# Kernel optimization log

Measured on AMD Instinct MI355X. Metric: run time of the kernel, lower is better.

Reference implementation:

```python
import jax, jax.numpy as jnp
import numpy as np

EMBED_DIM = 768
NUM_HEADS = 12
HEAD_DIM = EMBED_DIM // NUM_HEADS  # 64
SCALE = HEAD_DIM ** 0.5  # NOTE: source MULTIPLIES by sqrt(head_dim) (likely a bug, kept faithful)


def setup_inputs() -> dict:
    key = jax.random.key(0)
    kx, kq, kk, kv, ko = jax.random.split(key, 5)
    B, N, E = 8, 2048, EMBED_DIM
    s = 1.0 / np.sqrt(E)
    return {
        "x": jax.random.normal(kx, (B, N, E), dtype=jnp.float32),
        # nn.Linear weights stored [out_features, in_features], y = x @ W.T
        "Wq": jax.random.normal(kq, (E, E), dtype=jnp.float32) * s,
        "Wk": jax.random.normal(kk, (E, E), dtype=jnp.float32) * s,
        "Wv": jax.random.normal(kv, (E, E), dtype=jnp.float32) * s,
        "Wo": jax.random.normal(ko, (E, E), dtype=jnp.float32) * s,
    }


def reference(x, Wq, Wk, Wv, Wo):
    # Projections (no bias)
    q = jnp.einsum("bne,fe->bnf", x, Wq)
    k = jnp.einsum("bne,fe->bnf", x, Wk)
    v = jnp.einsum("bne,fe->bnf", x, Wv)
    # Full-width attention over the entire embedding dim (no head split, per source)
    energy = jnp.einsum("bid,bjd->bij", q, k) * SCALE  # [B, N, N]
    attn = jax.nn.softmax(energy, axis=-1)
    out = jnp.einsum("bij,bjd->bid", attn, v)  # [B, N, E]
    return jnp.einsum("bne,fe->bnf", out, Wo)
```

## Files before the change

kernel.cpp:

```cpp
#include <hip/hip_runtime.h>
#include <stdint.h>

typedef __bf16 bf16;
typedef __bf16 bf16x4 __attribute__((ext_vector_type(4)));
typedef __bf16 bf16x8 __attribute__((ext_vector_type(8)));
typedef float  f32x4  __attribute__((ext_vector_type(4)));

constexpr int BB = 8;
constexpr int NN = 2048;
constexpr int EE = 768;
constexpr int MM = BB * NN;
constexpr int E2 = 2 * EE;

typedef const __attribute__((address_space(1))) void* as1_cvp;
typedef __attribute__((address_space(3))) void* as3_vp;

static __device__ __forceinline__ void gld16(const void* g, void* l) {
  __builtin_amdgcn_global_load_lds((as1_cvp)g, (as3_vp)l, 16, 0, 0);
}

__global__ __launch_bounds__(256) void k_splitx(const float4* __restrict__ x,
                                                bf16x4* __restrict__ hi,
                                                bf16x4* __restrict__ lo, int n4) {
  int i = blockIdx.x * 256 + threadIdx.x;
  int st = gridDim.x * 256;
  for (; i < n4; i += st) {
    float4 v = x[i];
    bf16x4 h, l;
    h[0] = (bf16)v.x; l[0] = (bf16)(v.x - (float)h[0]);
    h[1] = (bf16)v.y; l[1] = (bf16)(v.y - (float)h[1]);
    h[2] = (bf16)v.z; l[2] = (bf16)(v.z - (float)h[2]);
    h[3] = (bf16)v.w; l[3] = (bf16)(v.w - (float)h[3]);
    hi[i] = h; lo[i] = l;
  }
}

__global__ __launch_bounds__(256) void k_wprep(const float4* __restrict__ wq,
                                               const float4* __restrict__ wk,
                                               const float4* __restrict__ wv,
                                               const float4* __restrict__ wo,
                                               bf16x4* __restrict__ qkh, bf16x4* __restrict__ qkl,
                                               bf16x4* __restrict__ vb,  bf16x4* __restrict__ ob) {
  const int n4 = EE * EE / 4;
  int sel = blockIdx.y;
  int i = blockIdx.x * 256 + threadIdx.x;
  int st = gridDim.x * 256;
  for (; i < n4; i += st) {
    if (sel <= 1) {
      float4 v = sel == 0 ? wq[i] : wk[i];
      bf16x4 h, l;
      h[0] = (bf16)v.x; l[0] = (bf16)(v.x - (float)h[0]);
      h[1] = (bf16)v.y; l[1] = (bf16)(v.y - (float)h[1]);
      h[2] = (bf16)v.z; l[2] = (bf16)(v.z - (float)h[2]);
      h[3] = (bf16)v.w; l[3] = (bf16)(v.w - (float)h[3]);
      int o = i + sel * n4;
      qkh[o] = h; qkl[o] = l;
    } else {
      float4 v = sel == 2 ? wv[i] : wo[i];
      bf16x4 h;
      h[0] = (bf16)v.x; h[1] = (bf16)v.y; h[2] = (bf16)v.z; h[3] = (bf16)v.w;
      if (sel == 2) vb[i] = h; else ob[i] = h;
    }
  }
}

template <bool SPLIT, int EPI>
__global__ __launch_bounds__(256, 2) void k_gemm(
    const bf16* __restrict__ Ah, const bf16* __restrict__ Al,
    const bf16* __restrict__ Bh, const bf16* __restrict__ Bl,
    void* __restrict__ C0, void* __restrict__ C1,
    int Kdim, int lda, int ldb, int ldc,
    long long sA, long long sB, long long sC, float cscale) {
  constexpr int NTILES = SPLIT ? 4 : 2;
  __shared__ __align__(16) bf16 sm[NTILES * 128 * 64];
  bf16* smAh = sm;
  bf16* smBh = sm + 128 * 64;
  bf16* smAl = SPLIT ? sm + 2 * 128 * 64 : nullptr;
  bf16* smBl = SPLIT ? sm + 3 * 128 * 64 : nullptr;

  const int tid = threadIdx.x;
  const int lane = tid & 63, wid = tid >> 6;
  const int lr = lane & 15, lq = lane >> 4;
  const int wr = (wid >> 1) * 64, wc = (wid & 1) * 64;
  const long long bz = blockIdx.z;
  const int col0 = blockIdx.x * 128, row0 = blockIdx.y * 128;

  const bf16* pAh = Ah + bz * sA;
  const bf16* pBh = Bh + bz * sB;
  const bf16* pAl = SPLIT ? (Al + bz * sA) : nullptr;
  const bf16* pBl = SPLIT ? (Bl + bz * sB) : nullptr;

  f32x4 acc[4][4] = {};

  for (int kt = 0; kt < Kdim; kt += 64) {
    {
      int o = tid * 16;
#pragma unroll
      for (int r = 0; r < 4; r++, o += 4096) {
        int row = o >> 7;
        int c = (o & 127) ^ ((row & 7) << 4);
        gld16((const char*)(pAh + (size_t)(row0 + row) * lda + kt) + c, (char*)smAh + o);
        gld16((const char*)(pBh + (size_t)(col0 + row) * ldb + kt) + c, (char*)smBh + o);
        if constexpr (SPLIT) {
          gld16((const char*)(pAl + (size_t)(row0 + row) * lda + kt) + c, (char*)smAl + o);
          gld16((const char*)(pBl + (size_t)(col0 + row) * ldb + kt) + c, (char*)smBl + o);
        }
      }
    }
    __syncthreads();
#pragma unroll
    for (int kk = 0; kk < 2; kk++) {
      bf16x8 ah[4], bh[4], al[4], bl[4];
#pragma unroll
      for (int i = 0; i < 4; i++) {
        int ar = wr + i * 16 + lr;
        int ao = ar * 128 + ((kk * 64 + lq * 16) ^ ((ar & 7) << 4));
        ah[i] = *(const bf16x8*)((const char*)smAh + ao);
        int br = wc + i * 16 + lr;
        int bo = br * 128 + ((kk * 64 + lq * 16) ^ ((br & 7) << 4));
        bh[i] = *(const bf16x8*)((const char*)smBh + bo);
        if constexpr (SPLIT) {
          al[i] = *(const bf16x8*)((const char*)smAl + ao);
          bl[i] = *(const bf16x8*)((const char*)smBl + bo);
        }
      }
#pragma unroll
      for (int i = 0; i < 4; i++)
#pragma unroll
        for (int j = 0; j < 4; j++) {
          acc[i][j] = __builtin_amdgcn_mfma_f32_16x16x32_bf16(ah[i], bh[j], acc[i][j], 0, 0, 0);
          if constexpr (SPLIT) {
            acc[i][j] = __builtin_amdgcn_mfma_f32_16x16x32_bf16(ah[i], bl[j], acc[i][j], 0, 0, 0);
            acc[i][j] = __builtin_amdgcn_mfma_f32_16x16x32_bf16(al[i], bh[j], acc[i][j], 0, 0, 0);
          }
        }
    }
    __syncthreads();
  }

#pragma unroll
  for (int i = 0; i < 4; i++) {
#pragma unroll
    for (int j2 = 0; j2 < 4; j2++) {
      f32x4 v = acc[i][j2];
      if constexpr (EPI == 3) {
        int r0 = row0 + wr + i * 16 + lq * 4;
        int c = col0 + wc + j2 * 16 + lr;
        int b = r0 >> 11, n0 = r0 & 2047;
        bf16x4 t;
#pragma unroll
        for (int j = 0; j < 4; j++) t[j] = (bf16)(v[j] * cscale);
        *(bf16x4*)((bf16*)C0 + ((size_t)b * EE + c) * NN + n0) = t;
      } else {
#pragma unroll
        for (int j = 0; j < 4; j++) {
          size_t r = (size_t)(row0 + wr + i * 16 + lq * 4 + j);
          size_t c = (size_t)(col0 + wc + j2 * 16 + lr);
          size_t idx = r * (size_t)ldc + c;
          float val = v[j] * cscale;
          if constexpr (EPI == 0) {
            bf16* Chp = (bf16*)C0 + bz * sC;
            bf16* Clp = (bf16*)C1 + bz * sC;
            bf16 h = (bf16)val;
            Chp[idx] = h;
            Clp[idx] = (bf16)(val - (float)h);
          } else if constexpr (EPI == 1) {
            float* Cp = (float*)C0 + bz * sC;
            Cp[idx] = val;
          } else {
            bf16* Cp = (bf16*)C0 + bz * sC;
            Cp[idx] = (bf16)val;
          }
        }
      }
    }
  }
}

__global__ __launch_bounds__(256) void k_softmax(float* __restrict__ S) {
  size_t row = blockIdx.x;
  float* srow = S + row * (size_t)NN;
  int tid = threadIdx.x;
  int wid = tid >> 6, lane = tid & 63;
  const float4* s4 = (const float4*)srow;
  float4 v0 = s4[tid * 2], v1 = s4[tid * 2 + 1];
  float vv[8] = {v0.x, v0.y, v0.z, v0.w, v1.x, v1.y, v1.z, v1.w};
  float m = vv[0];
#pragma unroll
  for (int j = 1; j < 8; j++) m = fmaxf(m, vv[j]);
#pragma unroll
  for (int d = 1; d < 64; d <<= 1) m = fmaxf(m, __shfl_xor(m, d));
  __shared__ float red[8];
  if (lane == 0) red[wid] = m;
  __syncthreads();
  m = fmaxf(fmaxf(red[0], red[1]), fmaxf(red[2], red[3]));
  float e[8];
  float ssum = 0.f;
#pragma unroll
  for (int j = 0; j < 8; j++) { e[j] = __expf(vv[j] - m); ssum += e[j]; }
#pragma unroll
  for (int d = 1; d < 64; d <<= 1) ssum += __shfl_xor(ssum, d);
  if (lane == 0) red[4 + wid] = ssum;
  __syncthreads();
  ssum = red[4] + red[5] + red[6] + red[7];
  float inv = 1.0f / ssum;
  bf16x8 p;
#pragma unroll
  for (int j = 0; j < 8; j++) p[j] = (bf16)(e[j] * inv);
  *(bf16x8*)((bf16*)srow + tid * 8) = p;
}

extern "C" void kernel_launch(void* const* d_in, const int* in_sizes, int n_in,
                              void* d_out, int out_size, void* d_ws, size_t ws_size,
                              hipStream_t stream) {
  const float* x  = (const float*)d_in[0];
  const float* Wq = (const float*)d_in[1];
  const float* Wk = (const float*)d_in[2];
  const float* Wv = (const float*)d_in[3];
  const float* Wo = (const float*)d_in[4];
  float* out = (float*)d_out;
  char* ws = (char*)d_ws;

  const size_t szXE = (size_t)MM * EE * 2;
  const size_t szWb = (size_t)EE * EE * 2;
  const size_t szQKh = (size_t)MM * E2 * 2;
  const size_t szS1 = (size_t)NN * NN * 4;

  bf16* xhi = (bf16*)(ws);
  bf16* xlo = (bf16*)(ws + szXE);
  char* wb  = ws + 2 * szXE;
  bf16* wqkh = (bf16*)(wb);
  bf16* wqkl = (bf16*)(wb + 2 * szWb);
  bf16* wvb  = (bf16*)(wb + 4 * szWb);
  bf16* wob  = (bf16*)(wb + 5 * szWb);
  char* qkb = wb + 6 * szWb;
  bf16* QKh = (bf16*)(qkb);
  bf16* QKl = (bf16*)(qkb + szQKh);
  bf16* Vt  = (bf16*)(qkb + 2 * szQKh);
  char* Sb  = qkb + 2 * szQKh + szXE;
  float* S  = (float*)Sb;
  bf16* Ao  = (bf16*)ws;

  size_t oS = (size_t)(Sb - ws);
  size_t avail = ws_size > oS ? ws_size - oS : 0;
  int G = 8;
  while (G > 1 && (size_t)G * szS1 > avail) G >>= 1;

  k_splitx<<<2048, 256, 0, stream>>>((const float4*)x, (bf16x4*)xhi, (bf16x4*)xlo, MM * EE / 4);
  k_wprep<<<dim3(144, 4), 256, 0, stream>>>((const float4*)Wq, (const float4*)Wk,
                                            (const float4*)Wv, (const float4*)Wo,
                                            (bf16x4*)wqkh, (bf16x4*)wqkl, (bf16x4*)wvb, (bf16x4*)wob);

  k_gemm<true, 0><<<dim3(E2 / 128, MM / 128, 1), 256, 0, stream>>>(
      xhi, xlo, wqkh, wqkl, QKh, QKl, EE, EE, EE, E2, 0, 0, 0, 1.0f);
  k_gemm<false, 3><<<dim3(EE / 128, MM / 128, 1), 256, 0, stream>>>(
      xhi, nullptr, wvb, nullptr, Vt, nullptr, EE, EE, EE, 0, 0, 0, 0, 1.0f);

  const long long sQK = (long long)NN * E2;
  for (int g = 0; g < BB; g += G) {
    const bf16* Qh = QKh + (size_t)g * NN * E2;
    const bf16* Ql = QKl + (size_t)g * NN * E2;
    k_gemm<true, 1><<<dim3(NN / 128, NN / 128, G), 256, 0, stream>>>(
        Qh, Ql, Qh + EE, Ql + EE, S, nullptr, EE, E2, E2, NN,
        sQK, sQK, (long long)NN * NN, 8.0f);
    k_softmax<<<G * NN, 256, 0, stream>>>(S);
    k_gemm<false, 2><<<dim3(EE / 128, NN / 128, G), 256, 0, stream>>>(
        (const bf16*)S, nullptr, Vt + (size_t)g * EE * NN, nullptr,
        Ao + (size_t)g * NN * EE, nullptr, NN, 2 * NN, NN, EE,
        2LL * NN * NN, (long long)EE * NN, (long long)NN * EE, 1.0f);
  }

  k_gemm<false, 1><<<dim3(EE / 128, MM / 128, 1), 256, 0, stream>>>(
      Ao, nullptr, wob, nullptr, out, nullptr, EE, EE, EE, EE, 0, 0, 0, 1.0f);
}
```

Baseline: 448.8 us.

## Template GEMM on K-tile and occupancy; compute V^T by operand swap

```diff
diff --git a/kernel.cpp b/kernel.cpp
--- a/kernel.cpp
+++ b/kernel.cpp
@@ -64,19 +64,21 @@
   }
 }
 
-template <bool SPLIT, int EPI>
-__global__ __launch_bounds__(256, 2) void k_gemm(
+template <bool SPLIT, int EPI, int BK, int LB>
+__global__ __launch_bounds__(256, LB) void k_gemm(
     const bf16* __restrict__ Ah, const bf16* __restrict__ Al,
     const bf16* __restrict__ Bh, const bf16* __restrict__ Bl,
     void* __restrict__ C0, void* __restrict__ C1,
     int Kdim, int lda, int ldb, int ldc,
     long long sA, long long sB, long long sC, float cscale) {
   constexpr int NTILES = SPLIT ? 4 : 2;
-  __shared__ __align__(16) bf16 sm[NTILES * 128 * 64];
-  bf16* smAh = sm;
-  bf16* smBh = sm + 128 * 64;
-  bf16* smAl = SPLIT ? sm + 2 * 128 * 64 : nullptr;
-  bf16* smBl = SPLIT ? sm + 3 * 128 * 64 : nullptr;
+  constexpr int ROWB = BK * 2;
+  constexpr int TILEB = 128 * ROWB;
+  __shared__ __align__(16) bf16 smm[NTILES * 128 * BK];
+  char* smAh = (char*)smm;
+  char* smBh = (char*)smm + TILEB;
+  char* smAl = SPLIT ? (char*)smm + 2 * TILEB : nullptr;
+  char* smBl = SPLIT ? (char*)smm + 3 * TILEB : nullptr;
 
   const int tid = threadIdx.x;
   const int lane = tid & 63, wid = tid >> 6;
@@ -92,36 +94,44 @@
 
   f32x4 acc[4][4] = {};
 
-  for (int kt = 0; kt < Kdim; kt += 64) {
+  for (int kt = 0; kt < Kdim; kt += BK) {
     {
       int o = tid * 16;
 #pragma unroll
-      for (int r = 0; r < 4; r++, o += 4096) {
-        int row = o >> 7;
-        int c = (o & 127) ^ ((row & 7) << 4);
-        gld16((const char*)(pAh + (size_t)(row0 + row) * lda + kt) + c, (char*)smAh + o);
-        gld16((const char*)(pBh + (size_t)(col0 + row) * ldb + kt) + c, (char*)smBh + o);
+      for (int r = 0; r < BK / 16; r++, o += 4096) {
+        int row = o / ROWB;
+        int c;
+        if constexpr (BK == 64) c = (o & (ROWB - 1)) ^ ((row & 7) << 4);
+        else                    c = (o & (ROWB - 1)) ^ (((row ^ (row >> 2)) & 3) << 4);
+        gld16((const char*)(pAh + (size_t)(row0 + row) * lda + kt) + c, smAh + o);
+        gld16((const char*)(pBh + (size_t)(col0 + row) * ldb + kt) + c, smBh + o);
         if constexpr (SPLIT) {
-          gld16((const char*)(pAl + (size_t)(row0 + row) * lda + kt) + c, (char*)smAl + o);
-          gld16((const char*)(pBl + (size_t)(col0 + row) * ldb + kt) + c, (char*)smBl + o);
+          gld16((const char*)(pAl + (size_t)(row0 + row) * lda + kt) + c, smAl + o);
+          gld16((const char*)(pBl + (size_t)(col0 + row) * ldb + kt) + c, smBl + o);
         }
       }
     }
     __syncthreads();
 #pragma unroll
-    for (int kk = 0; kk < 2; kk++) {
+    for (int kk = 0; kk < BK / 32; kk++) {
       bf16x8 ah[4], bh[4], al[4], bl[4];
 #pragma unroll
       for (int i = 0; i < 4; i++) {
         int ar = wr + i * 16 + lr;
-        int ao = ar * 128 + ((kk * 64 + lq * 16) ^ ((ar & 7) << 4));
-        ah[i] = *(const bf16x8*)((const char*)smAh + ao);
         int br = wc + i * 16 + lr;
-        int bo = br * 128 + ((kk * 64 + lq * 16) ^ ((br & 7) << 4));
-        bh[i] = *(const bf16x8*)((const char*)smBh + bo);
+        int ao, bo;
+        if constexpr (BK == 64) {
+          ao = ar * ROWB + ((kk * 64 + lq * 16) ^ ((ar & 7) << 4));
+          bo = br * ROWB + ((kk * 64 + lq * 16) ^ ((br & 7) << 4));
+        } else {
+          ao = ar * ROWB + ((lq * 16) ^ (((ar ^ (ar >> 2)) & 3) << 4));
+          bo = br * ROWB + ((lq * 16) ^ (((br ^ (br >> 2)) & 3) << 4));
+        }
+        ah[i] = *(const bf16x8*)(smAh + ao);
+        bh[i] = *(const bf16x8*)(smBh + bo);
         if constexpr (SPLIT) {
-          al[i] = *(const bf16x8*)((const char*)smAl + ao);
-          bl[i] = *(const bf16x8*)((const char*)smBl + bo);
+          al[i] = *(const bf16x8*)(smAl + ao);
+          bl[i] = *(const bf16x8*)(smBl + bo);
         }
       }
 #pragma unroll
@@ -143,34 +153,24 @@
 #pragma unroll
     for (int j2 = 0; j2 < 4; j2++) {
       f32x4 v = acc[i][j2];
-      if constexpr (EPI == 3) {
-        int r0 = row0 + wr + i * 16 + lq * 4;
-        int c = col0 + wc + j2 * 16 + lr;
-        int b = r0 >> 11, n0 = r0 & 2047;
-        bf16x4 t;
-#pragma unroll
-        for (int j = 0; j < 4; j++) t[j] = (bf16)(v[j] * cscale);
-        *(bf16x4*)((bf16*)C0 + ((size_t)b * EE + c) * NN + n0) = t;
-      } else {
-#pragma unroll
-        for (int j = 0; j < 4; j++) {
-          size_t r = (size_t)(row0 + wr + i * 16 + lq * 4 + j);
-          size_t c = (size_t)(col0 + wc + j2 * 16 + lr);
-          size_t idx = r * (size_t)ldc + c;
-          float val = v[j] * cscale;
-          if constexpr (EPI == 0) {
-            bf16* Chp = (bf16*)C0 + bz * sC;
-            bf16* Clp = (bf16*)C1 + bz * sC;
-            bf16 h = (bf16)val;
-            Chp[idx] = h;
-            Clp[idx] = (bf16)(val - (float)h);
-          } else if constexpr (EPI == 1) {
-            float* Cp = (float*)C0 + bz * sC;
-            Cp[idx] = val;
-          } else {
-            bf16* Cp = (bf16*)C0 + bz * sC;
-            Cp[idx] = (bf16)val;
-          }
+#pragma unroll
+      for (int j = 0; j < 4; j++) {
+        size_t r = (size_t)(row0 + wr + i * 16 + lq * 4 + j);
+        size_t c = (size_t)(col0 + wc + j2 * 16 + lr);
+        size_t idx = r * (size_t)ldc + c;
+        float val = v[j] * cscale;
+        if constexpr (EPI == 0) {
+          bf16* Chp = (bf16*)C0 + bz * sC;
+          bf16* Clp = (bf16*)C1 + bz * sC;
+          bf16 h = (bf16)val;
+          Chp[idx] = h;
+          Clp[idx] = (bf16)(val - (float)h);
+        } else if constexpr (EPI == 1) {
+          float* Cp = (float*)C0 + bz * sC;
+          Cp[idx] = val;
+        } else {
+          bf16* Cp = (bf16*)C0 + bz * sC;
+          Cp[idx] = (bf16)val;
         }
       }
     }
@@ -251,25 +251,25 @@
                                             (const float4*)Wv, (const float4*)Wo,
                                             (bf16x4*)wqkh, (bf16x4*)wqkl, (bf16x4*)wvb, (bf16x4*)wob);
 
-  k_gemm<true, 0><<<dim3(E2 / 128, MM / 128, 1), 256, 0, stream>>>(
+  k_gemm<true, 0, 64, 2><<<dim3(E2 / 128, MM / 128, 1), 256, 0, stream>>>(
       xhi, xlo, wqkh, wqkl, QKh, QKl, EE, EE, EE, E2, 0, 0, 0, 1.0f);
-  k_gemm<false, 3><<<dim3(EE / 128, MM / 128, 1), 256, 0, stream>>>(
-      xhi, nullptr, wvb, nullptr, Vt, nullptr, EE, EE, EE, 0, 0, 0, 0, 1.0f);
+  k_gemm<false, 2, 64, 4><<<dim3(MM / 128, EE / 128, 1), 256, 0, stream>>>(
+      wvb, nullptr, xhi, nullptr, Vt, nullptr, EE, EE, EE, MM, 0, 0, 0, 1.0f);
 
   const long long sQK = (long long)NN * E2;
   for (int g = 0; g < BB; g += G) {
     const bf16* Qh = QKh + (size_t)g * NN * E2;
     const bf16* Ql = QKl + (size_t)g * NN * E2;
-    k_gemm<true, 1><<<dim3(NN / 128, NN / 128, G), 256, 0, stream>>>(
+    k_gemm<true, 1, 32, 4><<<dim3(NN / 128, NN / 128, G), 256, 0, stream>>>(
         Qh, Ql, Qh + EE, Ql + EE, S, nullptr, EE, E2, E2, NN,
         sQK, sQK, (long long)NN * NN, 8.0f);
     k_softmax<<<G * NN, 256, 0, stream>>>(S);
-    k_gemm<false, 2><<<dim3(EE / 128, NN / 128, G), 256, 0, stream>>>(
-        (const bf16*)S, nullptr, Vt + (size_t)g * EE * NN, nullptr,
-        Ao + (size_t)g * NN * EE, nullptr, NN, 2 * NN, NN, EE,
-        2LL * NN * NN, (long long)EE * NN, (long long)NN * EE, 1.0f);
-  }
-
-  k_gemm<false, 1><<<dim3(EE / 128, MM / 128, 1), 256, 0, stream>>>(
+    k_gemm<false, 2, 64, 4><<<dim3(EE / 128, NN / 128, G), 256, 0, stream>>>(
+        (const bf16*)S, nullptr, Vt + (size_t)g * NN, nullptr,
+        Ao + (size_t)g * NN * EE, nullptr, NN, 2 * NN, MM, EE,
+        2LL * NN * NN, (long long)NN, (long long)NN * EE, 1.0f);
+  }
+
+  k_gemm<false, 1, 64, 4><<<dim3(EE / 128, MM / 128, 1), 256, 0, stream>>>(
       Ao, nullptr, wob, nullptr, out, nullptr, EE, EE, EE, EE, 0, 0, 0, 1.0f);
 }
```

After: 465.6 us. 3.7% more time.

## Fold output projection into V weights via precomputed Wo·Wv product

Applied to the files above, without the earlier changes.

```diff
diff --git a/kernel.cpp b/kernel.cpp
--- a/kernel.cpp
+++ b/kernel.cpp
@@ -37,10 +37,9 @@
 
 __global__ __launch_bounds__(256) void k_wprep(const float4* __restrict__ wq,
                                                const float4* __restrict__ wk,
-                                               const float4* __restrict__ wv,
                                                const float4* __restrict__ wo,
                                                bf16x4* __restrict__ qkh, bf16x4* __restrict__ qkl,
-                                               bf16x4* __restrict__ vb,  bf16x4* __restrict__ ob) {
+                                               bf16x4* __restrict__ ob) {
   const int n4 = EE * EE / 4;
   int sel = blockIdx.y;
   int i = blockIdx.x * 256 + threadIdx.x;
@@ -56,11 +55,35 @@
       int o = i + sel * n4;
       qkh[o] = h; qkl[o] = l;
     } else {
-      float4 v = sel == 2 ? wv[i] : wo[i];
+      float4 v = wo[i];
       bf16x4 h;
       h[0] = (bf16)v.x; h[1] = (bf16)v.y; h[2] = (bf16)v.z; h[3] = (bf16)v.w;
-      if (sel == 2) vb[i] = h; else ob[i] = h;
-    }
+      ob[i] = h;
+    }
+  }
+}
+
+__global__ __launch_bounds__(256) void k_wtrans(const float* __restrict__ src,
+                                                bf16* __restrict__ dst) {
+  __shared__ float t[64][65];
+  int e0 = blockIdx.x * 64, f0 = blockIdx.y * 64;
+  int tid = threadIdx.x;
+#pragma unroll
+  for (int h = 0; h < 4; h++) {
+    int lin = h * 1024 + tid * 4;
+    int r = lin >> 6, c = lin & 63;
+    float4 v = *(const float4*)(src + (size_t)(f0 + r) * EE + e0 + c);
+    t[r][c] = v.x; t[r][c + 1] = v.y; t[r][c + 2] = v.z; t[r][c + 3] = v.w;
+  }
+  __syncthreads();
+#pragma unroll
+  for (int h = 0; h < 4; h++) {
+    int lin = h * 1024 + tid * 4;
+    int er = lin >> 6, fc = lin & 63;
+    bf16x4 o;
+#pragma unroll
+    for (int j = 0; j < 4; j++) o[j] = (bf16)t[fc + j][er];
+    *(bf16x4*)(dst + (size_t)(e0 + er) * EE + f0 + fc) = o;
   }
 }
 
@@ -72,11 +95,11 @@
     int Kdim, int lda, int ldb, int ldc,
     long long sA, long long sB, long long sC, float cscale) {
   constexpr int NTILES = SPLIT ? 4 : 2;
-  __shared__ __align__(16) bf16 sm[NTILES * 128 * 64];
-  bf16* smAh = sm;
-  bf16* smBh = sm + 128 * 64;
-  bf16* smAl = SPLIT ? sm + 2 * 128 * 64 : nullptr;
-  bf16* smBl = SPLIT ? sm + 3 * 128 * 64 : nullptr;
+  __shared__ __align__(16) bf16 smm[NTILES * 128 * 64];
+  bf16* smAh = smm;
+  bf16* smBh = smm + 128 * 64;
+  bf16* smAl = SPLIT ? smm + 2 * 128 * 64 : nullptr;
+  bf16* smBl = SPLIT ? smm + 3 * 128 * 64 : nullptr;
 
   const int tid = threadIdx.x;
   const int lane = tid & 63, wid = tid >> 6;
@@ -143,34 +166,24 @@
 #pragma unroll
     for (int j2 = 0; j2 < 4; j2++) {
       f32x4 v = acc[i][j2];
-      if constexpr (EPI == 3) {
-        int r0 = row0 + wr + i * 16 + lq * 4;
-        int c = col0 + wc + j2 * 16 + lr;
-        int b = r0 >> 11, n0 = r0 & 2047;
-        bf16x4 t;
-#pragma unroll
-        for (int j = 0; j < 4; j++) t[j] = (bf16)(v[j] * cscale);
-        *(bf16x4*)((bf16*)C0 + ((size_t)b * EE + c) * NN + n0) = t;
-      } else {
-#pragma unroll
-        for (int j = 0; j < 4; j++) {
-          size_t r = (size_t)(row0 + wr + i * 16 + lq * 4 + j);
-          size_t c = (size_t)(col0 + wc + j2 * 16 + lr);
-          size_t idx = r * (size_t)ldc + c;
-          float val = v[j] * cscale;
-          if constexpr (EPI == 0) {
-            bf16* Chp = (bf16*)C0 + bz * sC;
-            bf16* Clp = (bf16*)C1 + bz * sC;
-            bf16 h = (bf16)val;
-            Chp[idx] = h;
-            Clp[idx] = (bf16)(val - (float)h);
-          } else if constexpr (EPI == 1) {
-            float* Cp = (float*)C0 + bz * sC;
-            Cp[idx] = val;
-          } else {
-            bf16* Cp = (bf16*)C0 + bz * sC;
-            Cp[idx] = (bf16)val;
-          }
+#pragma unroll
+      for (int j = 0; j < 4; j++) {
+        size_t r = (size_t)(row0 + wr + i * 16 + lq * 4 + j);
+        size_t c = (size_t)(col0 + wc + j2 * 16 + lr);
+        size_t idx = r * (size_t)ldc + c;
+        float val = v[j] * cscale;
+        if constexpr (EPI == 0) {
+          bf16* Chp = (bf16*)C0 + bz * sC;
+          bf16* Clp = (bf16*)C1 + bz * sC;
+          bf16 h = (bf16)val;
+          Chp[idx] = h;
+          Clp[idx] = (bf16)(val - (float)h);
+        } else if constexpr (EPI == 1) {
+          float* Cp = (float*)C0 + bz * sC;
+          Cp[idx] = val;
+        } else {
+          bf16* Cp = (bf16*)C0 + bz * sC;
+          Cp[idx] = (bf16)val;
         }
       }
     }
@@ -231,15 +244,15 @@
   char* wb  = ws + 2 * szXE;
   bf16* wqkh = (bf16*)(wb);
   bf16* wqkl = (bf16*)(wb + 2 * szWb);
-  bf16* wvb  = (bf16*)(wb + 4 * szWb);
+  bf16* wvT  = (bf16*)(wb + 4 * szWb);
   bf16* wob  = (bf16*)(wb + 5 * szWb);
-  char* qkb = wb + 6 * szWb;
+  bf16* wvob = (bf16*)(wb + 6 * szWb);
+  char* qkb = wb + 7 * szWb;
   bf16* QKh = (bf16*)(qkb);
   bf16* QKl = (bf16*)(qkb + szQKh);
-  bf16* Vt  = (bf16*)(qkb + 2 * szQKh);
+  bf16* Ut  = (bf16*)(qkb + 2 * szQKh);
   char* Sb  = qkb + 2 * szQKh + szXE;
   float* S  = (float*)Sb;
-  bf16* Ao  = (bf16*)ws;
 
   size_t oS = (size_t)(Sb - ws);
   size_t avail = ws_size > oS ? ws_size - oS : 0;
@@ -247,14 +260,17 @@
   while (G > 1 && (size_t)G * szS1 > avail) G >>= 1;
 
   k_splitx<<<2048, 256, 0, stream>>>((const float4*)x, (bf16x4*)xhi, (bf16x4*)xlo, MM * EE / 4);
-  k_wprep<<<dim3(144, 4), 256, 0, stream>>>((const float4*)Wq, (const float4*)Wk,
-                                            (const float4*)Wv, (const float4*)Wo,
-                                            (bf16x4*)wqkh, (bf16x4*)wqkl, (bf16x4*)wvb, (bf16x4*)wob);
+  k_wprep<<<dim3(144, 3), 256, 0, stream>>>((const float4*)Wq, (const float4*)Wk,
+                                            (const float4*)Wo,
+                                            (bf16x4*)wqkh, (bf16x4*)wqkl, (bf16x4*)wob);
+  k_wtrans<<<dim3(12, 12), 256, 0, stream>>>(Wv, wvT);
 
   k_gemm<true, 0><<<dim3(E2 / 128, MM / 128, 1), 256, 0, stream>>>(
       xhi, xlo, wqkh, wqkl, QKh, QKl, EE, EE, EE, E2, 0, 0, 0, 1.0f);
-  k_gemm<false, 3><<<dim3(EE / 128, MM / 128, 1), 256, 0, stream>>>(
-      xhi, nullptr, wvb, nullptr, Vt, nullptr, EE, EE, EE, 0, 0, 0, 0, 1.0f);
+  k_gemm<false, 2><<<dim3(EE / 128, EE / 128, 1), 256, 0, stream>>>(
+      wob, nullptr, wvT, nullptr, wvob, nullptr, EE, EE, EE, EE, 0, 0, 0, 1.0f);
+  k_gemm<false, 2><<<dim3(MM / 128, EE / 128, 1), 256, 0, stream>>>(
+      wvob, nullptr, xhi, nullptr, Ut, nullptr, EE, EE, EE, MM, 0, 0, 0, 1.0f);
 
   const long long sQK = (long long)NN * E2;
   for (int g = 0; g < BB; g += G) {
@@ -264,12 +280,9 @@
         Qh, Ql, Qh + EE, Ql + EE, S, nullptr, EE, E2, E2, NN,
         sQK, sQK, (long long)NN * NN, 8.0f);
     k_softmax<<<G * NN, 256, 0, stream>>>(S);
-    k_gemm<false, 2><<<dim3(EE / 128, NN / 128, G), 256, 0, stream>>>(
-        (const bf16*)S, nullptr, Vt + (size_t)g * EE * NN, nullptr,
-        Ao + (size_t)g * NN * EE, nullptr, NN, 2 * NN, NN, EE,
-        2LL * NN * NN, (long long)EE * NN, (long long)NN * EE, 1.0f);
-  }
-
-  k_gemm<false, 1><<<dim3(EE / 128, MM / 128, 1), 256, 0, stream>>>(
-      Ao, nullptr, wob, nullptr, out, nullptr, EE, EE, EE, EE, 0, 0, 0, 1.0f);
-}
+    k_gemm<false, 1><<<dim3(EE / 128, NN / 128, G), 256, 0, stream>>>(
+        (const bf16*)S, nullptr, Ut + (size_t)g * NN, nullptr,
+        out + (size_t)g * NN * EE, nullptr, NN, 2 * NN, MM, EE,
+        2LL * NN * NN, (long long)NN, (long long)NN * EE, 1.0f);
+  }
+}
```

Result: faster. 435.3 us (-3.0%).
